# Kernel tuning notes

Hardware: AMD Instinct MI355X
Metric: run time of the kernel (lower is better)

The kernel has to match this reference:

```python
import jax, jax.numpy as jnp
import numpy as np
from jax import lax

EPS = 1e-8
ROOT_2 = 1.41421
STYLE_SIZE = 512
OUT_CH = 512
STYLE_SCALE = (2.0 / STYLE_SIZE) ** 0.5   # Weight_Scaling(style_size): equalized-LR sqrt(2/fan_in)
OUT_SCALE = (2.0 / (OUT_CH * 1 * 1)) ** 0.5  # Weight_Scaling(out_channels*1*1)


def setup_inputs() -> dict:
    key = jax.random.key(0)
    ks = jax.random.split(key, 10)
    B, Cin, Cout, H, S = 8, 512, 512, 32, 512
    return {
        "x": jax.random.normal(ks[0], (B, Cin, H, H), dtype=jnp.float32),
        "style_base": jax.random.normal(ks[1], (B, S), dtype=jnp.float32),
        "noise": jax.random.normal(ks[2], (B, 1, 2 * H, 2 * H), dtype=jnp.float32),
        "t": jax.random.normal(ks[3], (B, Cout, 2 * H, 2 * H), dtype=jnp.float32),
        # learned params
        "affine_w": jax.random.normal(ks[4], (Cin, S), dtype=jnp.float32) * (1.0 / np.sqrt(S)),
        "affine_b": jnp.zeros((Cin,), dtype=jnp.float32),
        "conv_w": jax.random.normal(ks[5], (Cout, Cin, 3, 3), dtype=jnp.float32),
        "conv_b": jnp.zeros((1, Cout, 1, 1), dtype=jnp.float32),
        "prelu_a": jnp.asarray(0.25, dtype=jnp.float32),
        "noise_scalar": jnp.zeros((1, Cout, 1, 1), dtype=jnp.float32) + 0.1,
        "out_w": jax.random.normal(ks[6], (3, Cout, 1, 1), dtype=jnp.float32) * (1.0 / np.sqrt(Cout)),
        "out_b": jnp.zeros((3,), dtype=jnp.float32),
    }


def reference(x, style_base, noise, t, affine_w, affine_b, conv_w, conv_b,
              prelu_a, noise_scalar, out_w, out_b):
    B, Cin, H, W = x.shape
    # style_std = affine(Weight_Scaling(style_base)) + 1  -> [B, Cin]
    style_std = (style_base * STYLE_SCALE) @ affine_w.T + affine_b + 1.0

    # bilinear x2 upsample (align_corners=False == half-pixel, matches jax.image.resize)
    x = jax.image.resize(x, (B, Cin, 2 * H, 2 * W), method="bilinear")

    # modulated conv with L2 demodulation, expressed as input-scale + conv + output-scale
    # per-sample weight w_b[o,i,k,l] = w[o,i,k,l]*s[b,i] / ||w*s||_b,o
    wsq = jnp.sum(conv_w ** 2, axis=(2, 3))                      # [O, I]
    demod = 1.0 / jnp.sqrt(jnp.einsum("oi,bi->bo", wsq, style_std ** 2) + EPS)  # [B, O]
    xm = x * style_std[:, :, None, None]
    y = lax.conv_general_dilated(xm, conv_w, (1, 1), "SAME",
                                 dimension_numbers=("NCHW", "OIHW", "NCHW"))
    y = y * demod[:, :, None, None] + conv_b + noise_scalar * noise
    # PReLU (single shared slope)
    y = jnp.where(y >= 0, y, prelu_a * y)

    # out branch: skip add, scale, toRGB 1x1 conv, clamp
    y = (y + t) / ROOT_2
    out = lax.conv_general_dilated(y * OUT_SCALE, out_w, (1, 1), "SAME",
                                   dimension_numbers=("NCHW", "OIHW", "NCHW"))
    out = jnp.clip(out + out_b[None, :, None, None], 0.0, 1.0)
    return (y, out)
```

## Files before the change

kernel.cpp:

```cpp
#include <hip/hip_runtime.h>


typedef short bf16x8 __attribute__((ext_vector_type(8)));
typedef short short8v __attribute__((ext_vector_type(8)));
typedef float f32x16 __attribute__((ext_vector_type(16)));

#define WS_STYLE 0
#define WS_DEMOD 16384
#define WS_WSQ   32768
#define WS_WPACK 1081344
#define WS_XM    5799936

__device__ __forceinline__ short f2bf(float f) {
  unsigned u = __float_as_uint(f);
  u += 0x7FFFu + ((u >> 16) & 1u);
  return (short)(u >> 16);
}

__device__ __forceinline__ void gld16(const short* g, char* l) {
  __builtin_amdgcn_global_load_lds((const __attribute__((address_space(1))) void*)g,
                                   (__attribute__((address_space(3))) void*)l,
                                   16, 0, 0);
}

__global__ void k_style(const float* __restrict__ sb, const float* __restrict__ aw,
                        const float* __restrict__ ab, float* __restrict__ style) {
  __shared__ float s_sb[512];
  int b = blockIdx.x;
  for (int i = threadIdx.x; i < 512; i += 256) s_sb[i] = sb[b * 512 + i] * 0.0625f;
  __syncthreads();
  for (int i = threadIdx.x; i < 512; i += 256) {
    const float4* wrow = (const float4*)(aw + (size_t)i * 512);
    float acc = 0.f;
    #pragma unroll 4
    for (int s4 = 0; s4 < 128; ++s4) {
      float4 w4 = wrow[s4];
      float4 sv = *(const float4*)(s_sb + s4 * 4);
      acc += w4.x * sv.x + w4.y * sv.y + w4.z * sv.z + w4.w * sv.w;
    }
    style[b * 512 + i] = acc + ab[i] + 1.0f;
  }
}

__global__ void k_wsq(const float* __restrict__ cw, float* __restrict__ wsq) {
  int idx = blockIdx.x * 256 + threadIdx.x;
  const float* p = cw + (size_t)idx * 9;
  float s = 0.f;
  #pragma unroll
  for (int j = 0; j < 9; ++j) s += p[j] * p[j];
  wsq[idx] = s;
}

__global__ void k_demod(const float* __restrict__ wsq, const float* __restrict__ style,
                        float* __restrict__ demod) {
  int wid = threadIdx.x >> 6, lane = threadIdx.x & 63;
  int idx = blockIdx.x * 4 + wid;
  int b = idx >> 9, o = idx & 511;
  const float* wr = wsq + (size_t)o * 512;
  const float* ss = style + b * 512;
  float sum = 0.f;
  #pragma unroll
  for (int k = 0; k < 8; ++k) {
    int i = k * 64 + lane;
    float s = ss[i];
    sum += wr[i] * s * s;
  }
  #pragma unroll
  for (int off = 32; off; off >>= 1) sum += __shfl_down(sum, off);
  if (lane == 0) demod[b * 512 + o] = rsqrtf(sum + 1e-8f);
}

__global__ void k_upsample(const float* __restrict__ x, const float* __restrict__ style,
                           short* __restrict__ xm) {
  int b = blockIdx.x / 66, hp = blockIdx.x % 66;
  short* xmp = xm + ((size_t)b * 66 + hp) * 66 * 512;
  if (hp == 0 || hp == 65) {
    short8v z = {0, 0, 0, 0, 0, 0, 0, 0};
    for (int u = threadIdx.x; u < 66 * 512 / 8; u += 256) ((short8v*)xmp)[u] = z;
    return;
  }
  int h = hp - 1;
  int j0 = (h >> 1) - 1 + (h & 1);
  float fj = (h & 1) ? 0.25f : 0.75f;
  int j0c = j0 < 0 ? 0 : j0;
  int j1c = j0 + 1 > 31 ? 31 : j0 + 1;
  __shared__ float xt[2][64][33];
  int ccc = threadIdx.x & 63;
  int wsub = threadIdx.x >> 6;
  for (int c0 = 0; c0 < 512; c0 += 64) {
    __syncthreads();
    #pragma unroll 4
    for (int k = 0; k < 16; ++k) {
      int idx = k * 256 + threadIdx.x;
      int ii = idx & 31, cc = (idx >> 5) & 63, jj = idx >> 11;
      xt[jj][cc][ii] = x[(((size_t)b * 512 + c0 + cc) * 32 + (jj ? j1c : j0c)) * 32 + ii];
    }
    __syncthreads();
    float sstyle = style[b * 512 + c0 + ccc];
    #pragma unroll 4
    for (int wk = 0; wk < 16; ++wk) {
      int w = wk * 4 + wsub;
      int i0 = (w >> 1) - 1 + (w & 1);
      float fi = (w & 1) ? 0.25f : 0.75f;
      int i0c = i0 < 0 ? 0 : i0;
      int i1c = i0 + 1 > 31 ? 31 : i0 + 1;
      float v0 = xt[0][ccc][i0c] * (1.f - fi) + xt[0][ccc][i1c] * fi;
      float v1 = xt[1][ccc][i0c] * (1.f - fi) + xt[1][ccc][i1c] * fi;
      float v = (v0 * (1.f - fj) + v1 * fj) * sstyle;
      xmp[(size_t)(w + 1) * 512 + c0 + ccc] = f2bf(v);
    }
    if (wsub == 0) {
      xmp[c0 + ccc] = 0;
      xmp[(size_t)65 * 512 + c0 + ccc] = 0;
    }
  }
}

__global__ void k_packw(const float* __restrict__ cw, short* __restrict__ wpk) {
  int unit = blockIdx.x * 256 + threadIdx.x;
  int s = unit >> 11;
  int rem = unit & 2047;
  int o = rem >> 2, sp = rem & 3;
  int tap = s >> 4, cc = s & 15;
  int i0 = cc * 32 + ((sp ^ ((o >> 1) & 3)) << 3);
  const float* src = cw + ((size_t)o * 512 + i0) * 9 + tap;
  short8v v;
  #pragma unroll
  for (int j = 0; j < 8; ++j) v[j] = f2bf(src[j * 9]);
  *(short8v*)(wpk + (size_t)unit * 8) = v;
}

__global__ __launch_bounds__(512, 2) void k_conv(
    const short* __restrict__ xm, const short* __restrict__ wpk,
    const float* __restrict__ demod, const float* __restrict__ convb,
    const float* __restrict__ nscal, const float* __restrict__ noise,
    const float* __restrict__ t, const float* __restrict__ prelu_a,
    float* __restrict__ y) {
  __shared__ char WTs[3][32768];
  __shared__ char XMs[2][16896];

  int tid = threadIdx.x;
  int bid = blockIdx.x;
  int hpair = bid & 31, b = bid >> 5;
  int wid = tid >> 6, lane = tid & 63;
  int wo = wid & 3, wsrow = wid >> 2;
  int l31 = lane & 31, lg = lane >> 5;

  const short* xb = xm + ((size_t)b * 66 + hpair * 2) * 66 * 512;
  int wb0 = ((wo * 128 + l31) << 6) + ((lg ^ ((l31 >> 1) & 3)) << 4);

  int off0, off1, off2, d0, d1, d2;
  {
    int u = tid;
    int r = u / 264, rem = u - r * 264; int wp = rem >> 2, sp = rem & 3;
    off0 = (r * 66 + wp) * 512 + ((sp ^ ((wp >> 1) & 3)) << 3); d0 = u * 16;
    u = 512 + tid;
    r = u / 264; rem = u - r * 264; wp = rem >> 2; sp = rem & 3;
    off1 = (r * 66 + wp) * 512 + ((sp ^ ((wp >> 1) & 3)) << 3); d1 = u * 16;
    u = 1024 + (tid & 31);
    rem = u - 792;
    wp = rem >> 2; sp = rem & 3;
    off2 = (3 * 66 + wp) * 512 + ((sp ^ ((wp >> 1) & 3)) << 3); d2 = u * 16;
  }

  gld16(xb + off0, XMs[0] + d0);
  gld16(xb + off1, XMs[0] + d1);
  gld16(xb + off2, XMs[0] + d2);
  #pragma unroll
  for (int tt = 0; tt < 2; ++tt) {
    const short* ws = wpk + (size_t)(tt * 16) * 16384;
    #pragma unroll
    for (int j = 0; j < 4; ++j)
      gld16(ws + (j * 512 + tid) * 8, WTs[tt] + (j * 512 + tid) * 16);
  }

  f32x16 zf = {0,0,0,0,0,0,0,0,0,0,0,0,0,0,0,0};
  f32x16 acc[4][2];
  #pragma unroll
  for (int i = 0; i < 4; ++i) { acc[i][0] = zf; acc[i][1] = zf; }

  asm volatile("s_waitcnt vmcnt(0)" ::: "memory");
  __builtin_amdgcn_s_barrier();

  short8v xr0, xr1, xr2;

  #pragma unroll 1
  for (int cc = 0; cc < 16; ++cc) {
    const char* XMc = XMs[cc & 1];
    char* XMn = (char*)XMs[(cc & 1) ^ 1];
    #pragma unroll
    for (int tp = 0; tp < 9; ++tp) {
      const int kh = tp / 3, kw = tp % 3;

      if (!(cc == 15 && tp >= 7)) {
        const int ntap = (tp + 2) % 9;
        int ncc = cc + (tp >= 7 ? 1 : 0);
        const short* ws = wpk + (size_t)(ntap * 16 + ncc) * 16384;
        char* wd = (char*)WTs[(tp + 2) % 3];
        #pragma unroll
        for (int j = 0; j < 4; ++j)
          gld16(ws + (j * 512 + tid) * 8, wd + (j * 512 + tid) * 16);
      }
      asm volatile("" ::: "memory");
      if (tp == 0 && cc < 15) {
        const short* xs = xb + (cc + 1) * 32;
        xr0 = *(const short8v*)(xs + off0);
        xr1 = *(const short8v*)(xs + off1);
        xr2 = *(const short8v*)(xs + off2);
      }
      if (tp == 7 && cc < 15) {
        *(short8v*)(XMn + d0) = xr0;
        *(short8v*)(XMn + d1) = xr1;
        if (tid < 32) *(short8v*)(XMn + d2) = xr2;
      }

      const char* Wp = (const char*)WTs[tp % 3];
      bf16x8 wf0[4], wf1[4];
      #pragma unroll
      for (int cf = 0; cf < 4; ++cf) {
        wf0[cf] = *(const bf16x8*)(Wp + (wb0 + cf * 2048));
        wf1[cf] = *(const bf16x8*)(Wp + ((wb0 + cf * 2048) ^ 32));
      }
      int a = l31 + kw;
      int xo = ((wsrow + kh) * 66 + a) * 64 + ((lg ^ ((a >> 1) & 3)) << 4);
      bf16x8 xf00 = *(const bf16x8*)(XMc + xo);
      bf16x8 xf01 = *(const bf16x8*)(XMc + xo + 2048);
      bf16x8 xf10 = *(const bf16x8*)(XMc + (xo ^ 32));
      bf16x8 xf11 = *(const bf16x8*)(XMc + ((xo ^ 32) + 2048));

      __builtin_amdgcn_s_barrier();
      __builtin_amdgcn_s_setprio(1);
      acc[0][0] = __builtin_amdgcn_mfma_f32_32x32x16_bf16(wf0[0], xf00, acc[0][0], 0, 0, 0);
      acc[0][1] = __builtin_amdgcn_mfma_f32_32x32x16_bf16(wf0[0], xf01, acc[0][1], 0, 0, 0);
      acc[1][0] = __builtin_amdgcn_mfma_f32_32x32x16_bf16(wf0[1], xf00, acc[1][0], 0, 0, 0);
      acc[1][1] = __builtin_amdgcn_mfma_f32_32x32x16_bf16(wf0[1], xf01, acc[1][1], 0, 0, 0);
      acc[2][0] = __builtin_amdgcn_mfma_f32_32x32x16_bf16(wf0[2], xf00, acc[2][0], 0, 0, 0);
      acc[2][1] = __builtin_amdgcn_mfma_f32_32x32x16_bf16(wf0[2], xf01, acc[2][1], 0, 0, 0);
      acc[3][0] = __builtin_amdgcn_mfma_f32_32x32x16_bf16(wf0[3], xf00, acc[3][0], 0, 0, 0);
      acc[3][1] = __builtin_amdgcn_mfma_f32_32x32x16_bf16(wf0[3], xf01, acc[3][1], 0, 0, 0);
      acc[0][0] = __builtin_amdgcn_mfma_f32_32x32x16_bf16(wf1[0], xf10, acc[0][0], 0, 0, 0);
      acc[0][1] = __builtin_amdgcn_mfma_f32_32x32x16_bf16(wf1[0], xf11, acc[0][1], 0, 0, 0);
      acc[1][0] = __builtin_amdgcn_mfma_f32_32x32x16_bf16(wf1[1], xf10, acc[1][0], 0, 0, 0);
      acc[1][1] = __builtin_amdgcn_mfma_f32_32x32x16_bf16(wf1[1], xf11, acc[1][1], 0, 0, 0);
      acc[2][0] = __builtin_amdgcn_mfma_f32_32x32x16_bf16(wf1[2], xf10, acc[2][0], 0, 0, 0);
      acc[2][1] = __builtin_amdgcn_mfma_f32_32x32x16_bf16(wf1[2], xf11, acc[2][1], 0, 0, 0);
      acc[3][0] = __builtin_amdgcn_mfma_f32_32x32x16_bf16(wf1[3], xf10, acc[3][0], 0, 0, 0);
      acc[3][1] = __builtin_amdgcn_mfma_f32_32x32x16_bf16(wf1[3], xf11, acc[3][1], 0, 0, 0);
      __builtin_amdgcn_s_setprio(0);

      if (cc < 15) {
        if (tp <= 1)      asm volatile("s_waitcnt vmcnt(7)" ::: "memory");
        else if (tp == 8) asm volatile("s_waitcnt vmcnt(4) lgkmcnt(0)" ::: "memory");
        else              asm volatile("s_waitcnt vmcnt(4)" ::: "memory");
      } else {
        if (tp <= 6)      asm volatile("s_waitcnt vmcnt(4)" ::: "memory");
        else              asm volatile("s_waitcnt vmcnt(0) lgkmcnt(0)" ::: "memory");
      }
      __builtin_amdgcn_s_barrier();
    }
  }

  float pa = prelu_a[0];
  const float inv_r2 = 1.0f / 1.41421f;
  int h = hpair * 2 + wsrow;
  float nz0 = noise[((size_t)b * 64 + h) * 64 + l31];
  float nz1 = noise[((size_t)b * 64 + h) * 64 + 32 + l31];
  #pragma unroll
  for (int cf = 0; cf < 4; ++cf) {
    #pragma unroll
    for (int reg = 0; reg < 16; ++reg) {
      int orow = (reg & 3) + 8 * (reg >> 2) + 4 * lg;
      int o = wo * 128 + cf * 32 + orow;
      float dm = demod[b * 512 + o];
      float cb = convb[o];
      float ns = nscal[o];
      #pragma unroll
      for (int sf = 0; sf < 2; ++sf) {
        int w = sf * 32 + l31;
        float v = acc[cf][sf][reg];
        v = v * dm + cb + ns * (sf ? nz1 : nz0);
        v = (v >= 0.f) ? v : pa * v;
        size_t oi = (((size_t)b * 512 + o) * 64 + h) * 64 + w;
        v = (v + t[oi]) * inv_r2;
        y[oi] = v;
      }
    }
  }
}

__global__ void k_rgb(const float* __restrict__ y, const float* __restrict__ ow,
                      const float* __restrict__ ob, float* __restrict__ out) {
  int b = blockIdx.x >> 6, h = blockIdx.x & 63;
  int w = threadIdx.x & 63, g = threadIdx.x >> 6;
  const float* yb = y + (((size_t)b * 512) * 64 + h) * 64 + w;
  float s0 = 0.f, s1 = 0.f, s2 = 0.f;
  for (int o = g * 128; o < g * 128 + 128; ++o) {
    float v = yb[(size_t)o * 4096];
    s0 += v * ow[o];
    s1 += v * ow[512 + o];
    s2 += v * ow[1024 + o];
  }
  __shared__ float red[3][4][64];
  red[0][g][w] = s0; red[1][g][w] = s1; red[2][g][w] = s2;
  __syncthreads();
  if (threadIdx.x < 192) {
    int c = threadIdx.x >> 6, ww = threadIdx.x & 63;
    float s = red[c][0][ww] + red[c][1][ww] + red[c][2][ww] + red[c][3][ww];
    s = s * 0.0625f + ob[c];
    s = fminf(fmaxf(s, 0.f), 1.f);
    out[(((size_t)b * 3 + c) * 64 + h) * 64 + ww] = s;
  }
}

extern "C" void kernel_launch(void* const* d_in, const int* in_sizes, int n_in,
                              void* d_out, int out_size, void* d_ws, size_t ws_size,
                              hipStream_t stream) {
  const float* x     = (const float*)d_in[0];
  const float* sb    = (const float*)d_in[1];
  const float* noise = (const float*)d_in[2];
  const float* t     = (const float*)d_in[3];
  const float* aw    = (const float*)d_in[4];
  const float* ab    = (const float*)d_in[5];
  const float* cw    = (const float*)d_in[6];
  const float* cb    = (const float*)d_in[7];
  const float* pa    = (const float*)d_in[8];
  const float* ns    = (const float*)d_in[9];
  const float* ow    = (const float*)d_in[10];
  const float* ob    = (const float*)d_in[11];
  char* ws = (char*)d_ws;
  float* style = (float*)(ws + WS_STYLE);
  float* demod = (float*)(ws + WS_DEMOD);
  float* wsq   = (float*)(ws + WS_WSQ);
  short* wpk   = (short*)(ws + WS_WPACK);
  short* xmw   = (short*)(ws + WS_XM);
  float* y   = (float*)d_out;
  float* out = y + 16777216;

  k_style<<<8, 256, 0, stream>>>(sb, aw, ab, style);
  k_wsq<<<1024, 256, 0, stream>>>(cw, wsq);
  k_demod<<<1024, 256, 0, stream>>>(wsq, style, demod);
  k_upsample<<<528, 256, 0, stream>>>(x, style, xmw);
  k_packw<<<1152, 256, 0, stream>>>(cw, wpk);
  k_conv<<<256, 512, 0, stream>>>(xmw, wpk, demod, cb, ns, noise, t, pa, y);
  k_rgb<<<512, 256, 0, stream>>>(y, ow, ob, out);
}
```

Baseline: 265.0 us.

## Halve conv block to 4 waves, each computing two output rows

Reshapes the modulated-conv kernel from 8 waves (4 channel groups × 2 rows) to 4 waves that each compute both output rows. Each loaded weight fragment is then reused across twice as many MFMAs, which roughly halves LDS weight reads per MFMA. The next input tile is now staged with async global-to-LDS loads instead of register round-trips, and the per-tap waitcnt schedule is simplified. In exchange each wave holds twice the accumulators (256 fp32 regs), and the CU runs fewer waves, so latency hiding may suffer.

```diff
diff --git a/kernel.cpp b/kernel.cpp
--- a/kernel.cpp
+++ b/kernel.cpp
@@ -130,7 +130,7 @@
   *(short8v*)(wpk + (size_t)unit * 8) = v;
 }
 
-__global__ __launch_bounds__(512, 2) void k_conv(
+__global__ __launch_bounds__(256, 1) void k_conv(
     const short* __restrict__ xm, const short* __restrict__ wpk,
     const float* __restrict__ demod, const float* __restrict__ convb,
     const float* __restrict__ nscal, const float* __restrict__ noise,
@@ -142,47 +142,50 @@
   int tid = threadIdx.x;
   int bid = blockIdx.x;
   int hpair = bid & 31, b = bid >> 5;
-  int wid = tid >> 6, lane = tid & 63;
-  int wo = wid & 3, wsrow = wid >> 2;
+  int wo = tid >> 6, lane = tid & 63;
   int l31 = lane & 31, lg = lane >> 5;
 
   const short* xb = xm + ((size_t)b * 66 + hpair * 2) * 66 * 512;
   int wb0 = ((wo * 128 + l31) << 6) + ((lg ^ ((l31 >> 1) & 3)) << 4);
 
-  int off0, off1, off2, d0, d1, d2;
+  int xoff[5], xdst[5];
+  #pragma unroll
+  for (int k = 0; k < 4; ++k) {
+    int u = k * 256 + tid;
+    int r = u / 264, rem = u - r * 264;
+    int wp = rem >> 2, sp = rem & 3;
+    xoff[k] = (r * 66 + wp) * 512 + ((sp ^ ((wp >> 1) & 3)) << 3);
+    xdst[k] = u * 16;
+  }
   {
-    int u = tid;
-    int r = u / 264, rem = u - r * 264; int wp = rem >> 2, sp = rem & 3;
-    off0 = (r * 66 + wp) * 512 + ((sp ^ ((wp >> 1) & 3)) << 3); d0 = u * 16;
-    u = 512 + tid;
-    r = u / 264; rem = u - r * 264; wp = rem >> 2; sp = rem & 3;
-    off1 = (r * 66 + wp) * 512 + ((sp ^ ((wp >> 1) & 3)) << 3); d1 = u * 16;
-    u = 1024 + (tid & 31);
-    rem = u - 792;
-    wp = rem >> 2; sp = rem & 3;
-    off2 = (3 * 66 + wp) * 512 + ((sp ^ ((wp >> 1) & 3)) << 3); d2 = u * 16;
-  }
-
-  gld16(xb + off0, XMs[0] + d0);
-  gld16(xb + off1, XMs[0] + d1);
-  gld16(xb + off2, XMs[0] + d2);
+    int u = 1024 + (tid & 31);
+    int rem = u - 792;
+    int wp = rem >> 2, sp = rem & 3;
+    xoff[4] = (3 * 66 + wp) * 512 + ((sp ^ ((wp >> 1) & 3)) << 3);
+    xdst[4] = u * 16;
+  }
+
+  #pragma unroll
+  for (int k = 0; k < 4; ++k) gld16(xb + xoff[k], XMs[0] + xdst[k]);
+  if (tid < 32) gld16(xb + xoff[4], XMs[0] + xdst[4]);
   #pragma unroll
   for (int tt = 0; tt < 2; ++tt) {
     const short* ws = wpk + (size_t)(tt * 16) * 16384;
     #pragma unroll
-    for (int j = 0; j < 4; ++j)
-      gld16(ws + (j * 512 + tid) * 8, WTs[tt] + (j * 512 + tid) * 16);
+    for (int j = 0; j < 8; ++j)
+      gld16(ws + (j * 256 + tid) * 8, WTs[tt] + (j * 256 + tid) * 16);
   }
 
   f32x16 zf = {0,0,0,0,0,0,0,0,0,0,0,0,0,0,0,0};
-  f32x16 acc[4][2];
-  #pragma unroll
-  for (int i = 0; i < 4; ++i) { acc[i][0] = zf; acc[i][1] = zf; }
+  f32x16 acc[4][2][2];
+  #pragma unroll
+  for (int i = 0; i < 4; ++i)
+    #pragma unroll
+    for (int j = 0; j < 2; ++j) { acc[i][j][0] = zf; acc[i][j][1] = zf; }
 
   asm volatile("s_waitcnt vmcnt(0)" ::: "memory");
   __builtin_amdgcn_s_barrier();
-
-  short8v xr0, xr1, xr2;
+  __builtin_amdgcn_sched_barrier(0);
 
   #pragma unroll 1
   for (int cc = 0; cc < 16; ++cc) {
@@ -198,20 +201,14 @@
         const short* ws = wpk + (size_t)(ntap * 16 + ncc) * 16384;
         char* wd = (char*)WTs[(tp + 2) % 3];
         #pragma unroll
-        for (int j = 0; j < 4; ++j)
-          gld16(ws + (j * 512 + tid) * 8, wd + (j * 512 + tid) * 16);
-      }
-      asm volatile("" ::: "memory");
+        for (int j = 0; j < 8; ++j)
+          gld16(ws + (j * 256 + tid) * 8, wd + (j * 256 + tid) * 16);
+      }
       if (tp == 0 && cc < 15) {
         const short* xs = xb + (cc + 1) * 32;
-        xr0 = *(const short8v*)(xs + off0);
-        xr1 = *(const short8v*)(xs + off1);
-        xr2 = *(const short8v*)(xs + off2);
-      }
-      if (tp == 7 && cc < 15) {
-        *(short8v*)(XMn + d0) = xr0;
-        *(short8v*)(XMn + d1) = xr1;
-        if (tid < 32) *(short8v*)(XMn + d2) = xr2;
+        #pragma unroll
+        for (int k = 0; k < 4; ++k) gld16(xs + xoff[k], XMn + xdst[k]);
+        if (tid < 32) gld16(xs + xoff[4], XMn + xdst[4]);
       }
 
       const char* Wp = (const char*)WTs[tp % 3];
@@ -222,49 +219,47 @@
         wf1[cf] = *(const bf16x8*)(Wp + ((wb0 + cf * 2048) ^ 32));
       }
       int a = l31 + kw;
-      int xo = ((wsrow + kh) * 66 + a) * 64 + ((lg ^ ((a >> 1) & 3)) << 4);
-      bf16x8 xf00 = *(const bf16x8*)(XMc + xo);
-      bf16x8 xf01 = *(const bf16x8*)(XMc + xo + 2048);
-      bf16x8 xf10 = *(const bf16x8*)(XMc + (xo ^ 32));
-      bf16x8 xf11 = *(const bf16x8*)(XMc + ((xo ^ 32) + 2048));
-
+      int swz = (lg ^ ((a >> 1) & 3)) << 4;
+      bf16x8 xf0[2][2], xf1[2][2];
+      #pragma unroll
+      for (int rr = 0; rr < 2; ++rr) {
+        int xo = ((rr + kh) * 66 + a) * 64 + swz;
+        xf0[rr][0] = *(const bf16x8*)(XMc + xo);
+        xf0[rr][1] = *(const bf16x8*)(XMc + xo + 2048);
+        xf1[rr][0] = *(const bf16x8*)(XMc + (xo ^ 32));
+        xf1[rr][1] = *(const bf16x8*)(XMc + ((xo ^ 32) + 2048));
+      }
+
+      __builtin_amdgcn_s_setprio(1);
+      #pragma unroll
+      for (int cf = 0; cf < 4; ++cf)
+        #pragma unroll
+        for (int rr = 0; rr < 2; ++rr)
+          #pragma unroll
+          for (int sf = 0; sf < 2; ++sf)
+            acc[cf][rr][sf] = __builtin_amdgcn_mfma_f32_32x32x16_bf16(
+                wf0[cf], xf0[rr][sf], acc[cf][rr][sf], 0, 0, 0);
+      #pragma unroll
+      for (int cf = 0; cf < 4; ++cf)
+        #pragma unroll
+        for (int rr = 0; rr < 2; ++rr)
+          #pragma unroll
+          for (int sf = 0; sf < 2; ++sf)
+            acc[cf][rr][sf] = __builtin_amdgcn_mfma_f32_32x32x16_bf16(
+                wf1[cf], xf1[rr][sf], acc[cf][rr][sf], 0, 0, 0);
+      __builtin_amdgcn_s_setprio(0);
+
+      if (cc == 15 && tp >= 7)
+        asm volatile("s_waitcnt vmcnt(0)" ::: "memory");
+      else
+        asm volatile("s_waitcnt vmcnt(8)" ::: "memory");
       __builtin_amdgcn_s_barrier();
-      __builtin_amdgcn_s_setprio(1);
-      acc[0][0] = __builtin_amdgcn_mfma_f32_32x32x16_bf16(wf0[0], xf00, acc[0][0], 0, 0, 0);
-      acc[0][1] = __builtin_amdgcn_mfma_f32_32x32x16_bf16(wf0[0], xf01, acc[0][1], 0, 0, 0);
-      acc[1][0] = __builtin_amdgcn_mfma_f32_32x32x16_bf16(wf0[1], xf00, acc[1][0], 0, 0, 0);
-      acc[1][1] = __builtin_amdgcn_mfma_f32_32x32x16_bf16(wf0[1], xf01, acc[1][1], 0, 0, 0);
-      acc[2][0] = __builtin_amdgcn_mfma_f32_32x32x16_bf16(wf0[2], xf00, acc[2][0], 0, 0, 0);
-      acc[2][1] = __builtin_amdgcn_mfma_f32_32x32x16_bf16(wf0[2], xf01, acc[2][1], 0, 0, 0);
-      acc[3][0] = __builtin_amdgcn_mfma_f32_32x32x16_bf16(wf0[3], xf00, acc[3][0], 0, 0, 0);
-      acc[3][1] = __builtin_amdgcn_mfma_f32_32x32x16_bf16(wf0[3], xf01, acc[3][1], 0, 0, 0);
-      acc[0][0] = __builtin_amdgcn_mfma_f32_32x32x16_bf16(wf1[0], xf10, acc[0][0], 0, 0, 0);
-      acc[0][1] = __builtin_amdgcn_mfma_f32_32x32x16_bf16(wf1[0], xf11, acc[0][1], 0, 0, 0);
-      acc[1][0] = __builtin_amdgcn_mfma_f32_32x32x16_bf16(wf1[1], xf10, acc[1][0], 0, 0, 0);
-      acc[1][1] = __builtin_amdgcn_mfma_f32_32x32x16_bf16(wf1[1], xf11, acc[1][1], 0, 0, 0);
-      acc[2][0] = __builtin_amdgcn_mfma_f32_32x32x16_bf16(wf1[2], xf10, acc[2][0], 0, 0, 0);
-      acc[2][1] = __builtin_amdgcn_mfma_f32_32x32x16_bf16(wf1[2], xf11, acc[2][1], 0, 0, 0);
-      acc[3][0] = __builtin_amdgcn_mfma_f32_32x32x16_bf16(wf1[3], xf10, acc[3][0], 0, 0, 0);
-      acc[3][1] = __builtin_amdgcn_mfma_f32_32x32x16_bf16(wf1[3], xf11, acc[3][1], 0, 0, 0);
-      __builtin_amdgcn_s_setprio(0);
-
-      if (cc < 15) {
-        if (tp <= 1)      asm volatile("s_waitcnt vmcnt(7)" ::: "memory");
-        else if (tp == 8) asm volatile("s_waitcnt vmcnt(4) lgkmcnt(0)" ::: "memory");
-        else              asm volatile("s_waitcnt vmcnt(4)" ::: "memory");
-      } else {
-        if (tp <= 6)      asm volatile("s_waitcnt vmcnt(4)" ::: "memory");
-        else              asm volatile("s_waitcnt vmcnt(0) lgkmcnt(0)" ::: "memory");
-      }
-      __builtin_amdgcn_s_barrier();
+      __builtin_amdgcn_sched_barrier(0);
     }
   }
 
   float pa = prelu_a[0];
   const float inv_r2 = 1.0f / 1.41421f;
-  int h = hpair * 2 + wsrow;
-  float nz0 = noise[((size_t)b * 64 + h) * 64 + l31];
-  float nz1 = noise[((size_t)b * 64 + h) * 64 + 32 + l31];
   #pragma unroll
   for (int cf = 0; cf < 4; ++cf) {
     #pragma unroll
@@ -275,14 +270,18 @@
       float cb = convb[o];
       float ns = nscal[o];
       #pragma unroll
-      for (int sf = 0; sf < 2; ++sf) {
-        int w = sf * 32 + l31;
-        float v = acc[cf][sf][reg];
-        v = v * dm + cb + ns * (sf ? nz1 : nz0);
-        v = (v >= 0.f) ? v : pa * v;
-        size_t oi = (((size_t)b * 512 + o) * 64 + h) * 64 + w;
-        v = (v + t[oi]) * inv_r2;
-        y[oi] = v;
+      for (int rr = 0; rr < 2; ++rr) {
+        int h = hpair * 2 + rr;
+        #pragma unroll
+        for (int sf = 0; sf < 2; ++sf) {
+          int w = sf * 32 + l31;
+          float v = acc[cf][rr][sf][reg];
+          v = v * dm + cb + ns * noise[((size_t)b * 64 + h) * 64 + w];
+          v = (v >= 0.f) ? v : pa * v;
+          size_t oi = (((size_t)b * 512 + o) * 64 + h) * 64 + w;
+          v = (v + t[oi]) * inv_r2;
+          y[oi] = v;
+        }
       }
     }
   }
@@ -341,6 +340,6 @@
   k_demod<<<1024, 256, 0, stream>>>(wsq, style, demod);
   k_upsample<<<528, 256, 0, stream>>>(x, style, xmw);
   k_packw<<<1152, 256, 0, stream>>>(cw, wpk);
-  k_conv<<<256, 512, 0, stream>>>(xmw, wpk, demod, cb, ns, noise, t, pa, y);
+  k_conv<<<256, 256, 0, stream>>>(xmw, wpk, demod, cb, ns, noise, t, pa, y);
   k_rgb<<<512, 256, 0, stream>>>(y, ow, ob, out);
 }
```

After: 305.7 us. +15.3%, slower.

## Retile conv blocks to 4 rows x 256 channels with per-kernel-row weight stages

Applied to the files above, without the earlier changes.

Each block now covers 4 output rows and half of the output channels instead of 2 rows and all 512 channels. Weights are staged one kernel row (3 taps) at a time into a double buffer, cutting the barrier count per channel chunk from 9 to 3. The input halo is now loaded directly into LDS with async global_load_lds instead of through registers. This improves reuse of the input tile and lowers sync overhead, but every stage waits for vmcnt(0), which removes the finer overlap the old wait counts gave, and LDS use rises to about 148KB, which probably drops occupancy to one block per CU.

```diff
diff --git a/kernel.cpp b/kernel.cpp
--- a/kernel.cpp
+++ b/kernel.cpp
@@ -136,42 +136,38 @@
     const float* __restrict__ nscal, const float* __restrict__ noise,
     const float* __restrict__ t, const float* __restrict__ prelu_a,
     float* __restrict__ y) {
-  __shared__ char WTs[3][32768];
-  __shared__ char XMs[2][16896];
+  __shared__ char WTs[2][49152];
+  __shared__ char XMs[2][25344];
 
   int tid = threadIdx.x;
   int bid = blockIdx.x;
-  int hpair = bid & 31, b = bid >> 5;
+  int cohalf = bid & 1, hq = (bid >> 1) & 15, b = bid >> 5;
   int wid = tid >> 6, lane = tid & 63;
-  int wo = wid & 3, wsrow = wid >> 2;
+  int wo = wid & 1, wsrow = wid >> 1;
   int l31 = lane & 31, lg = lane >> 5;
 
-  const short* xb = xm + ((size_t)b * 66 + hpair * 2) * 66 * 512;
+  const short* xb = xm + ((size_t)b * 66 + hq * 4) * 66 * 512;
+  const short* wpkh = wpk + (size_t)cohalf * 256 * 32;
   int wb0 = ((wo * 128 + l31) << 6) + ((lg ^ ((l31 >> 1) & 3)) << 4);
 
-  int off0, off1, off2, d0, d1, d2;
-  {
-    int u = tid;
-    int r = u / 264, rem = u - r * 264; int wp = rem >> 2, sp = rem & 3;
-    off0 = (r * 66 + wp) * 512 + ((sp ^ ((wp >> 1) & 3)) << 3); d0 = u * 16;
-    u = 512 + tid;
-    r = u / 264; rem = u - r * 264; wp = rem >> 2; sp = rem & 3;
-    off1 = (r * 66 + wp) * 512 + ((sp ^ ((wp >> 1) & 3)) << 3); d1 = u * 16;
-    u = 1024 + (tid & 31);
-    rem = u - 792;
-    wp = rem >> 2; sp = rem & 3;
-    off2 = (3 * 66 + wp) * 512 + ((sp ^ ((wp >> 1) & 3)) << 3); d2 = u * 16;
-  }
-
-  gld16(xb + off0, XMs[0] + d0);
-  gld16(xb + off1, XMs[0] + d1);
-  gld16(xb + off2, XMs[0] + d2);
-  #pragma unroll
-  for (int tt = 0; tt < 2; ++tt) {
-    const short* ws = wpk + (size_t)(tt * 16) * 16384;
-    #pragma unroll
-    for (int j = 0; j < 4; ++j)
-      gld16(ws + (j * 512 + tid) * 8, WTs[tt] + (j * 512 + tid) * 16);
+  #pragma unroll
+  for (int k = 0; k < 3; ++k) {
+    int u = k * 512 + tid;
+    int r = u / 264, rem = u - r * 264;
+    int wp = rem >> 2, sp = rem & 3;
+    gld16(xb + (size_t)(r * 66 + wp) * 512 + ((sp ^ ((wp >> 1) & 3)) << 3), XMs[0] + u * 16);
+  }
+  if (tid < 48) {
+    int u = 1536 + tid;
+    int rem = u - 1320;
+    int wp = rem >> 2, sp = rem & 3;
+    gld16(xb + (size_t)(5 * 66 + wp) * 512 + ((sp ^ ((wp >> 1) & 3)) << 3), XMs[0] + u * 16);
+  }
+  #pragma unroll
+  for (int j = 0; j < 3; ++j) {
+    const short* ws = wpkh + (size_t)(j * 16) * 16384;
+    gld16(ws + tid * 8, WTs[0] + j * 16384 + tid * 16);
+    gld16(ws + (512 + tid) * 8, WTs[0] + j * 16384 + (512 + tid) * 16);
   }
 
   f32x16 zf = {0,0,0,0,0,0,0,0,0,0,0,0,0,0,0,0};
@@ -181,88 +177,82 @@
 
   asm volatile("s_waitcnt vmcnt(0)" ::: "memory");
   __builtin_amdgcn_s_barrier();
-
-  short8v xr0, xr1, xr2;
+  __builtin_amdgcn_sched_barrier(0);
 
   #pragma unroll 1
   for (int cc = 0; cc < 16; ++cc) {
     const char* XMc = XMs[cc & 1];
     char* XMn = (char*)XMs[(cc & 1) ^ 1];
     #pragma unroll
-    for (int tp = 0; tp < 9; ++tp) {
-      const int kh = tp / 3, kw = tp % 3;
-
-      if (!(cc == 15 && tp >= 7)) {
-        const int ntap = (tp + 2) % 9;
-        int ncc = cc + (tp >= 7 ? 1 : 0);
-        const short* ws = wpk + (size_t)(ntap * 16 + ncc) * 16384;
-        char* wd = (char*)WTs[(tp + 2) % 3];
-        #pragma unroll
-        for (int j = 0; j < 4; ++j)
-          gld16(ws + (j * 512 + tid) * 8, wd + (j * 512 + tid) * 16);
+    for (int krow = 0; krow < 3; ++krow) {
+      int g = cc * 3 + krow;
+      const char* WTc = WTs[g & 1];
+      char* WTn = (char*)WTs[(g & 1) ^ 1];
+
+      if (g < 47) {
+        int nkrow = (krow < 2) ? krow + 1 : 0;
+        int ncc = (krow < 2) ? cc : cc + 1;
+        #pragma unroll
+        for (int j = 0; j < 3; ++j) {
+          const short* ws = wpkh + (size_t)((nkrow * 3 + j) * 16 + ncc) * 16384;
+          gld16(ws + tid * 8, WTn + j * 16384 + tid * 16);
+          gld16(ws + (512 + tid) * 8, WTn + j * 16384 + (512 + tid) * 16);
+        }
       }
-      asm volatile("" ::: "memory");
-      if (tp == 0 && cc < 15) {
+      if (krow == 0 && cc < 15) {
         const short* xs = xb + (cc + 1) * 32;
-        xr0 = *(const short8v*)(xs + off0);
-        xr1 = *(const short8v*)(xs + off1);
-        xr2 = *(const short8v*)(xs + off2);
+        #pragma unroll
+        for (int k = 0; k < 3; ++k) {
+          int u = k * 512 + tid;
+          int r = u / 264, rem = u - r * 264;
+          int wp = rem >> 2, sp = rem & 3;
+          gld16(xs + (size_t)(r * 66 + wp) * 512 + ((sp ^ ((wp >> 1) & 3)) << 3), XMn + u * 16);
+        }
+        if (tid < 48) {
+          int u = 1536 + tid;
+          int rem = u - 1320;
+          int wp = rem >> 2, sp = rem & 3;
+          gld16(xs + (size_t)(5 * 66 + wp) * 512 + ((sp ^ ((wp >> 1) & 3)) << 3), XMn + u * 16);
+        }
       }
-      if (tp == 7 && cc < 15) {
-        *(short8v*)(XMn + d0) = xr0;
-        *(short8v*)(XMn + d1) = xr1;
-        if (tid < 32) *(short8v*)(XMn + d2) = xr2;
+
+      #pragma unroll
+      for (int j = 0; j < 3; ++j) {
+        const char* Wp = WTc + j * 16384;
+        bf16x8 wf0[4], wf1[4];
+        #pragma unroll
+        for (int cf = 0; cf < 4; ++cf) {
+          wf0[cf] = *(const bf16x8*)(Wp + (wb0 + cf * 2048));
+          wf1[cf] = *(const bf16x8*)(Wp + ((wb0 + cf * 2048) ^ 32));
+        }
+        int a = l31 + j;
+        int xo = ((wsrow + krow) * 66 + a) * 64 + ((lg ^ ((a >> 1) & 3)) << 4);
+        bf16x8 xf00 = *(const bf16x8*)(XMc + xo);
+        bf16x8 xf01 = *(const bf16x8*)(XMc + xo + 2048);
+        bf16x8 xf10 = *(const bf16x8*)(XMc + (xo ^ 32));
+        bf16x8 xf11 = *(const bf16x8*)(XMc + ((xo ^ 32) + 2048));
+
+        #pragma unroll
+        for (int cf = 0; cf < 4; ++cf) {
+          acc[cf][0] = __builtin_amdgcn_mfma_f32_32x32x16_bf16(wf0[cf], xf00, acc[cf][0], 0, 0, 0);
+          acc[cf][1] = __builtin_amdgcn_mfma_f32_32x32x16_bf16(wf0[cf], xf01, acc[cf][1], 0, 0, 0);
+        }
+        #pragma unroll
+        for (int cf = 0; cf < 4; ++cf) {
+          acc[cf][0] = __builtin_amdgcn_mfma_f32_32x32x16_bf16(wf1[cf], xf10, acc[cf][0], 0, 0, 0);
+          acc[cf][1] = __builtin_amdgcn_mfma_f32_32x32x16_bf16(wf1[cf], xf11, acc[cf][1], 0, 0, 0);
+        }
       }
 
-      const char* Wp = (const char*)WTs[tp % 3];
-      bf16x8 wf0[4], wf1[4];
-      #pragma unroll
-      for (int cf = 0; cf < 4; ++cf) {
-        wf0[cf] = *(const bf16x8*)(Wp + (wb0 + cf * 2048));
-        wf1[cf] = *(const bf16x8*)(Wp + ((wb0 + cf * 2048) ^ 32));
-      }
-      int a = l31 + kw;
-      int xo = ((wsrow + kh) * 66 + a) * 64 + ((lg ^ ((a >> 1) & 3)) << 4);
-      bf16x8 xf00 = *(const bf16x8*)(XMc + xo);
-      bf16x8 xf01 = *(const bf16x8*)(XMc + xo + 2048);
-      bf16x8 xf10 = *(const bf16x8*)(XMc + (xo ^ 32));
-      bf16x8 xf11 = *(const bf16x8*)(XMc + ((xo ^ 32) + 2048));
-
+      asm volatile("s_waitcnt vmcnt(0)" ::: "memory");
       __builtin_amdgcn_s_barrier();
-      __builtin_amdgcn_s_setprio(1);
-      acc[0][0] = __builtin_amdgcn_mfma_f32_32x32x16_bf16(wf0[0], xf00, acc[0][0], 0, 0, 0);
-      acc[0][1] = __builtin_amdgcn_mfma_f32_32x32x16_bf16(wf0[0], xf01, acc[0][1], 0, 0, 0);
-      acc[1][0] = __builtin_amdgcn_mfma_f32_32x32x16_bf16(wf0[1], xf00, acc[1][0], 0, 0, 0);
-      acc[1][1] = __builtin_amdgcn_mfma_f32_32x32x16_bf16(wf0[1], xf01, acc[1][1], 0, 0, 0);
-      acc[2][0] = __builtin_amdgcn_mfma_f32_32x32x16_bf16(wf0[2], xf00, acc[2][0], 0, 0, 0);
-      acc[2][1] = __builtin_amdgcn_mfma_f32_32x32x16_bf16(wf0[2], xf01, acc[2][1], 0, 0, 0);
-      acc[3][0] = __builtin_amdgcn_mfma_f32_32x32x16_bf16(wf0[3], xf00, acc[3][0], 0, 0, 0);
-      acc[3][1] = __builtin_amdgcn_mfma_f32_32x32x16_bf16(wf0[3], xf01, acc[3][1], 0, 0, 0);
-      acc[0][0] = __builtin_amdgcn_mfma_f32_32x32x16_bf16(wf1[0], xf10, acc[0][0], 0, 0, 0);
-      acc[0][1] = __builtin_amdgcn_mfma_f32_32x32x16_bf16(wf1[0], xf11, acc[0][1], 0, 0, 0);
-      acc[1][0] = __builtin_amdgcn_mfma_f32_32x32x16_bf16(wf1[1], xf10, acc[1][0], 0, 0, 0);
-      acc[1][1] = __builtin_amdgcn_mfma_f32_32x32x16_bf16(wf1[1], xf11, acc[1][1], 0, 0, 0);
-      acc[2][0] = __builtin_amdgcn_mfma_f32_32x32x16_bf16(wf1[2], xf10, acc[2][0], 0, 0, 0);
-      acc[2][1] = __builtin_amdgcn_mfma_f32_32x32x16_bf16(wf1[2], xf11, acc[2][1], 0, 0, 0);
-      acc[3][0] = __builtin_amdgcn_mfma_f32_32x32x16_bf16(wf1[3], xf10, acc[3][0], 0, 0, 0);
-      acc[3][1] = __builtin_amdgcn_mfma_f32_32x32x16_bf16(wf1[3], xf11, acc[3][1], 0, 0, 0);
-      __builtin_amdgcn_s_setprio(0);
-
-      if (cc < 15) {
-        if (tp <= 1)      asm volatile("s_waitcnt vmcnt(7)" ::: "memory");
-        else if (tp == 8) asm volatile("s_waitcnt vmcnt(4) lgkmcnt(0)" ::: "memory");
-        else              asm volatile("s_waitcnt vmcnt(4)" ::: "memory");
-      } else {
-        if (tp <= 6)      asm volatile("s_waitcnt vmcnt(4)" ::: "memory");
-        else              asm volatile("s_waitcnt vmcnt(0) lgkmcnt(0)" ::: "memory");
-      }
-      __builtin_amdgcn_s_barrier();
+      __builtin_amdgcn_sched_barrier(0);
     }
   }
 
   float pa = prelu_a[0];
   const float inv_r2 = 1.0f / 1.41421f;
-  int h = hpair * 2 + wsrow;
+  int h = hq * 4 + wsrow;
   float nz0 = noise[((size_t)b * 64 + h) * 64 + l31];
   float nz1 = noise[((size_t)b * 64 + h) * 64 + 32 + l31];
   #pragma unroll
@@ -270,7 +260,7 @@
     #pragma unroll
     for (int reg = 0; reg < 16; ++reg) {
       int orow = (reg & 3) + 8 * (reg >> 2) + 4 * lg;
-      int o = wo * 128 + cf * 32 + orow;
+      int o = cohalf * 256 + wo * 128 + cf * 32 + orow;
       float dm = demod[b * 512 + o];
       float cb = convb[o];
       float ns = nscal[o];
```

New measurement: 227.1 us. 1.17x faster.
